# Performance work log

Measured on AMD Instinct MI355X. Metric: run time of the kernel, lower is better.

## Reference

```python
import jax, jax.numpy as jnp
import numpy as np

B, S, H, NH = 8, 1024, 1024, 16
HD = H // NH


def setup_inputs() -> dict:
    key = jax.random.key(0)
    ks = jax.random.split(key, 9)
    scale = 0.02
    d = {"x": jax.random.normal(ks[0], (B, S, H), jnp.float32)}
    for i, n in enumerate(["q", "k", "v", "o"]):
        d["W" + n] = jax.random.normal(ks[1 + i], (H, H), jnp.float32) * scale
        d["b" + n] = jnp.zeros((H,), jnp.float32)
    d["position_idx"] = jnp.arange(S, dtype=jnp.int32).reshape(1, S)
    return d


def _rotate_half(x):
    x1, x2 = jnp.split(x, 2, axis=-1)
    return jnp.concatenate([-x2, x1], axis=-1)


def _apply_rope(x, position_idx):
    # Faithful to source (precedence bug included): (10000**arange) / head_dim
    inv_freq = 1.0 / (10000.0 ** jnp.arange(0, HD, 2, dtype=jnp.float32) / HD)
    freqs = jnp.einsum('bi,j->bij', position_idx.astype(jnp.float32), inv_freq)  # [1,S,HD/2]
    emb = jnp.concatenate([freqs, freqs], axis=-1)  # [1,S,HD]
    cos = jnp.cos(emb).reshape(1, 1, -1, HD)
    sin = jnp.sin(emb).reshape(1, 1, -1, HD)
    return x * cos + _rotate_half(x) * sin


def reference(x, Wq, bq, Wk, bk, Wv, bv, Wo, bo, position_idx):
    b, s, _ = x.shape

    def to_heads(t):  # [b,s,H] -> [b,nh,s,hd]
        return t.reshape(b, s, NH, HD).transpose(0, 2, 1, 3)

    q = to_heads(x @ Wq + bq)
    k = to_heads(x @ Wk + bk)
    v = to_heads(x @ Wv + bv)
    q = _apply_rope(q, position_idx)
    k = _apply_rope(k, position_idx)
    scores = jnp.einsum('bhqd,bhkd->bhqk', q, k) / jnp.sqrt(jnp.float32(HD))
    attn = jax.nn.softmax(scores, axis=-1)
    out = jnp.einsum('bhqk,bhkd->bhqd', attn, v)  # [b,nh,s,hd]
    out = out.transpose(0, 2, 1, 3).reshape(b, s, NH * HD)
    return out @ Wo + bo
```

## Files before the change

### kernel.cpp

```cpp
#include <hip/hip_runtime.h>
#include <hip/hip_bf16.h>
#include <math.h>

#define B_  8
#define S_  1024
#define H_  1024
#define NH_ 16
#define HD_ 64
#define M_  (B_*S_)
#define K_  1024

typedef __hip_bfloat16 bf16;
typedef __attribute__((ext_vector_type(8))) short  short8;
typedef __attribute__((ext_vector_type(4))) short  short4v;
typedef __attribute__((ext_vector_type(8))) __bf16 bf16x8;
typedef __attribute__((ext_vector_type(4))) float  f32x4;

#define MFMA16(a, b, c) __builtin_amdgcn_mfma_f32_16x16x32_bf16((a), (b), (c), 0, 0, 0)
#define QSCALE 0.18033688011112042f

static __device__ __forceinline__ short f2bf_s(float f) {
  unsigned u = __float_as_uint(f);
  u += 0x7fffu + ((u >> 16) & 1u);
  return (short)(u >> 16);
}
static __device__ __forceinline__ float bf2f_s(short s) {
  return __uint_as_float((unsigned)(unsigned short)s << 16);
}

static __device__ __forceinline__ void gload16(const void* g, void* l) {
  __builtin_amdgcn_global_load_lds(
      (const __attribute__((address_space(1))) void*)g,
      (__attribute__((address_space(3))) void*)l, 16, 0, 0);
}

__global__ __launch_bounds__(256) void convert_x_kernel(const float* __restrict__ x,
                                                        short* __restrict__ xb) {
  int i = blockIdx.x * 256 + threadIdx.x;
  size_t base = (size_t)i * 8;
  f32x4 a = *(const f32x4*)(x + base);
  f32x4 b = *(const f32x4*)(x + base + 4);
  short8 v;
  #pragma unroll
  for (int j = 0; j < 4; ++j) { v[j] = f2bf_s(a[j]); v[4 + j] = f2bf_s(b[j]); }
  *(short8*)(xb + base) = v;
}

__global__ void ingest_bias_kernel(const float* __restrict__ b0, const float* __restrict__ b1,
                                   const float* __restrict__ b2, const float* __restrict__ b3,
                                   short* __restrict__ bbuf) {
  int i = blockIdx.x * 256 + threadIdx.x;
  if (i >= 4096) return;
  const float* src = (i < 1024) ? b0 : (i < 2048) ? b1 : (i < 3072) ? b2 : b3;
  bbuf[i] = f2bf_s(src[i & 1023]);
}

__global__ void rope_tables_kernel(const int* __restrict__ pos,
                                   float* __restrict__ cost, float* __restrict__ sint) {
  int i = blockIdx.x * blockDim.x + threadIdx.x;
  if (i >= S_ * 32) return;
  int s = i >> 5, f = i & 31;
  double inv = 64.0 / pow(10000.0, (double)(2 * f));
  double ang = (double)pos[s] * inv;
  cost[i] = (float)cos(ang);
  sint[i] = (float)sin(ang);
}

__global__ __launch_bounds__(256) void transpose_w_kernel(
    const float* __restrict__ w0, const float* __restrict__ w1,
    const float* __restrict__ w2, const float* __restrict__ w3,
    bf16* __restrict__ outbase) {
  const float* src = (blockIdx.y == 0) ? w0 : (blockIdx.y == 1) ? w1 : (blockIdx.y == 2) ? w2 : w3;
  short* dst = (short*)outbase + (size_t)blockIdx.y * H_ * H_;
  __shared__ short tile[64][72];
  const int t = threadIdx.x;
  const int tr = blockIdx.x >> 4, tc = blockIdx.x & 15;
  const int r0 = tr * 64, c0 = tc * 64;
  #pragma unroll
  for (int p = 0; p < 2; ++p) {
    int row = p * 32 + (t >> 3);
    int c8  = (t & 7) * 8;
    const float* f = src + (size_t)(r0 + row) * H_ + c0 + c8;
    #pragma unroll
    for (int j = 0; j < 8; ++j) tile[c8 + j][row] = f2bf_s(f[j]);
  }
  __syncthreads();
  #pragma unroll
  for (int p = 0; p < 2; ++p) {
    int row = p * 32 + (t >> 3);
    int c8  = (t & 7) * 8;
    short8 v;
    #pragma unroll
    for (int j = 0; j < 8; ++j) v[j] = tile[row][c8 + j];
    *(short8*)(dst + (size_t)(c0 + row) * H_ + r0 + c8) = v;
  }
}

__global__ __launch_bounds__(256) void gemm_bt_kernel(
    const bf16* __restrict__ A, const bf16* __restrict__ Bt, const short* __restrict__ bias,
    void* __restrict__ C, const float* __restrict__ cost, const float* __restrict__ sint,
    int mode, float qscale) {
  __shared__ short sA[128 * 32];
  __shared__ short sB[128 * 32];
  const int t  = threadIdx.x;
  const int bm = blockIdx.y * 128, bn = blockIdx.x * 128;
  const int lane = t & 63, wid = t >> 6;
  const int wr = wid >> 1, wc = wid & 1;
  const int lm = lane & 15, lg = lane >> 4;
  f32x4 acc[4][4] = {};

  const short* Ag = (const short*)A;
  const short* Bg = (const short*)Bt;

  for (int k0 = 0; k0 < K_; k0 += 32) {
    #pragma unroll
    for (int c = 0; c < 2; ++c) {
      int flat = c * 256 + t;
      int row = flat >> 2, k8 = (flat & 3) * 8;
      gload16(Ag + (size_t)(bm + row) * K_ + k0 + k8, sA + flat * 8);
      gload16(Bg + (size_t)(bn + row) * K_ + k0 + k8, sB + flat * 8);
    }
    __syncthreads();
    bf16x8 af[4], bfr[4];
    #pragma unroll
    for (int i = 0; i < 4; ++i) af[i]  = *(const bf16x8*)(sA + (wr * 64 + i * 16 + lm) * 32 + lg * 8);
    #pragma unroll
    for (int j = 0; j < 4; ++j) bfr[j] = *(const bf16x8*)(sB + (wc * 64 + j * 16 + lm) * 32 + lg * 8);
    #pragma unroll
    for (int i = 0; i < 4; ++i)
      #pragma unroll
      for (int j = 0; j < 4; ++j)
        acc[i][j] = MFMA16(af[i], bfr[j], acc[i][j]);
    __syncthreads();
  }

  if (mode == 0) {
    #pragma unroll
    for (int i = 0; i < 4; ++i) {
      int row = bm + wr * 64 + i * 16 + lg * 4;
      #pragma unroll
      for (int j = 0; j < 4; ++j) {
        int col = bn + wc * 64 + j * 16 + lm;
        float bv = bf2f_s(bias[col]);
        #pragma unroll
        for (int r = 0; r < 4; ++r)
          ((float*)C)[(size_t)(row + r) * H_ + col] = acc[i][j][r] + bv;
      }
    }
  } else if (mode == 1) {
    #pragma unroll
    for (int i = 0; i < 4; ++i) {
      int row = bm + wr * 64 + i * 16 + lg * 4;
      #pragma unroll
      for (int j = 0; j < 2; ++j) {
        int col0 = bn + wc * 64 + j * 16 + lm;
        int d = col0 & 63;
        float b0 = bf2f_s(bias[col0]);
        float b1 = bf2f_s(bias[col0 + 32]);
        #pragma unroll
        for (int r = 0; r < 4; ++r) {
          int s = (row + r) & (S_ - 1);
          float cv = cost[s * 32 + d] * qscale, sv = sint[s * 32 + d] * qscale;
          float x1 = acc[i][j][r] + b0;
          float x2 = acc[i][j + 2][r] + b1;
          ((short*)C)[(size_t)(row + r) * H_ + col0]      = f2bf_s(x1 * cv - x2 * sv);
          ((short*)C)[(size_t)(row + r) * H_ + col0 + 32] = f2bf_s(x2 * cv + x1 * sv);
        }
      }
    }
  } else {
    #pragma unroll
    for (int i = 0; i < 4; ++i) {
      int row = bm + wr * 64 + i * 16 + lg * 4;
      int bb = row >> 10;
      int sb = row & 1023;
      int pos = (sb & ~31) | (((sb >> 2) & 3) << 3) | (((sb >> 4) & 1) << 2);
      #pragma unroll
      for (int j = 0; j < 4; ++j) {
        int col = bn + wc * 64 + j * 16 + lm;
        int colv = col & 1023;
        float bv = bf2f_s(bias[col]);
        short4v pk;
        #pragma unroll
        for (int r = 0; r < 4; ++r) pk[r] = f2bf_s(acc[i][j][r] + bv);
        short* dstp = (short*)C + ((size_t)(bb * NH_ + (colv >> 6)) * HD_ + (colv & 63)) * S_ + pos;
        *(short4v*)dstp = pk;
      }
    }
  }
}

__global__ __launch_bounds__(256) void attn_kernel(
    const bf16* __restrict__ q, const bf16* __restrict__ k,
    const bf16* __restrict__ vt, bf16* __restrict__ o) {
  const int bh = blockIdx.x, b = bh >> 4, h = bh & 15;
  const int t = threadIdx.x, wid = t >> 6, lane = t & 63;
  const int lm = lane & 15, lg = lane >> 4;
  const int qw = blockIdx.y * 128 + wid * 32;

  __shared__ short sK[2][32 * 64];
  __shared__ short sV[2][64 * 32];

  const int keyr = t >> 3, ccK = t & 7, tcK = ccK ^ (keyr & 7);
  const int dr   = t >> 2, ccV = t & 3, tcV = ccV ^ (dr & 3);
  const short* ksrc = (const short*)k + (size_t)(b * S_ + keyr) * H_ + h * HD_ + tcK * 8;
  const short* vsrc = (const short*)vt + (size_t)bh * HD_ * S_ + (size_t)dr * S_ + tcV * 8;

  const int kO0 = lm * 64 + ((lg ^ (lm & 7)) << 3);
  const int kO1 = lm * 64 + (((4 + lg) ^ (lm & 7)) << 3);
  const int vO  = lm * 32 + ((lg ^ (lm & 3)) << 3);

  const short* qbase = (const short*)q + (size_t)(b * S_ + qw) * H_ + h * HD_;
  bf16x8 qf[2][2];
  #pragma unroll
  for (int mi = 0; mi < 2; ++mi)
    #pragma unroll
    for (int dh = 0; dh < 2; ++dh)
      qf[mi][dh] = *(const bf16x8*)(qbase + (size_t)(mi * 16 + lm) * H_ + dh * 32 + lg * 8);

  float ps[2] = {0.f, 0.f};
  f32x4 oacc[2][4] = {};

  gload16(ksrc, sK[0] + t * 8);
  gload16(vsrc, sV[0] + t * 8);
  __syncthreads();

  int cur = 0;
  for (int kk = 0; kk < S_; kk += 32) {
    if (kk + 32 < S_) {
      gload16(ksrc + (size_t)(kk + 32) * H_, sK[cur ^ 1] + t * 8);
      gload16(vsrc + (kk + 32), sV[cur ^ 1] + t * 8);
    }
    const short* sKc = sK[cur];
    const short* sVc = sV[cur];

    f32x4 sc[2][2] = {};
    #pragma unroll
    for (int nt = 0; nt < 2; ++nt) {
      bf16x8 kf0 = *(const bf16x8*)(sKc + nt * 16 * 64 + kO0);
      bf16x8 kf1 = *(const bf16x8*)(sKc + nt * 16 * 64 + kO1);
      #pragma unroll
      for (int mi = 0; mi < 2; ++mi) {
        sc[mi][nt] = MFMA16(kf0, qf[mi][0], sc[mi][nt]);
        sc[mi][nt] = MFMA16(kf1, qf[mi][1], sc[mi][nt]);
      }
    }
    bf16x8 vf[4];
    #pragma unroll
    for (int dt = 0; dt < 4; ++dt)
      vf[dt] = *(const bf16x8*)(sVc + dt * 16 * 32 + vO);

    bf16x8 pf[2];
    #pragma unroll
    for (int mi = 0; mi < 2; ++mi)
      #pragma unroll
      for (int nt = 0; nt < 2; ++nt)
        #pragma unroll
        for (int r = 0; r < 4; ++r) {
          float p = exp2f(fminf(sc[mi][nt][r], 115.0f));
          ps[mi] += p;
          pf[mi][nt * 4 + r] = (__bf16)p;
        }
    #pragma unroll
    for (int mi = 0; mi < 2; ++mi)
      #pragma unroll
      for (int dt = 0; dt < 4; ++dt)
        oacc[mi][dt] = MFMA16(pf[mi], vf[dt], oacc[mi][dt]);

    __syncthreads();
    cur ^= 1;
  }
  #pragma unroll
  for (int mi = 0; mi < 2; ++mi) {
    ps[mi] += __shfl_xor(ps[mi], 16);
    ps[mi] += __shfl_xor(ps[mi], 32);
  }
  #pragma unroll
  for (int mi = 0; mi < 2; ++mi) {
    #pragma unroll
    for (int r = 0; r < 4; ++r) {
      float rr = 1.0f / __shfl(ps[mi], lg * 4 + r);
      int row = qw + mi * 16 + lg * 4 + r;
      #pragma unroll
      for (int dt = 0; dt < 4; ++dt) {
        int col = h * HD_ + dt * 16 + lm;
        ((short*)o)[(size_t)(b * S_ + row) * H_ + col] = f2bf_s(oacc[mi][dt][r] * rr);
      }
    }
  }
}

extern "C" void kernel_launch(void* const* d_in, const int* in_sizes, int n_in,
                              void* d_out, int out_size, void* d_ws, size_t ws_size,
                              hipStream_t stream) {
  (void)out_size; (void)ws_size;
  int ix, iWq, iWk, iWv, iWo, ibq, ibk, ibv, ibo, ipos;
  const int XS = 8388608, WS = 1048576;
  if (n_in == 10 && in_sizes[0] == WS && in_sizes[9] == XS) {
    iWk = 0; iWo = 1; iWq = 2; iWv = 3; ibk = 4; ibo = 5; ibq = 6; ibv = 7; ipos = 8; ix = 9;
  } else if (n_in == 10 && in_sizes[0] == 1024 && in_sizes[9] == XS) {
    ipos = 0; ibo = 1; iWo = 2; ibv = 3; iWv = 4; ibk = 5; iWk = 6; ibq = 7; iWq = 8; ix = 9;
  } else if (n_in == 10 && in_sizes[0] == XS && in_sizes[1] == 1024) {
    ix = 0; ipos = 1; ibv = 2; ibq = 3; ibo = 4; ibk = 5; iWv = 6; iWq = 7; iWo = 8; iWk = 9;
  } else {
    ix = 0; iWq = 1; ibq = 2; iWk = 3; ibk = 4; iWv = 5; ibv = 6; iWo = 7; ibo = 8; ipos = 9;
  }
  const float* x  = (const float*)d_in[ix];
  const float* Wq = (const float*)d_in[iWq];
  const float* bq = (const float*)d_in[ibq];
  const float* Wk = (const float*)d_in[iWk];
  const float* bk = (const float*)d_in[ibk];
  const float* Wv = (const float*)d_in[iWv];
  const float* bv = (const float*)d_in[ibv];
  const float* Wo = (const float*)d_in[iWo];
  const float* bo = (const float*)d_in[ibo];
  const int*  pos = (const int*)d_in[ipos];

  char* ws = (char*)d_ws;
  bf16* wt    = (bf16*)(ws);
  bf16* kb    = (bf16*)(ws + (8ull  << 20));
  bf16* vtb   = (bf16*)(ws + (24ull << 20));
  bf16* obuf  = (bf16*)(ws + (40ull << 20));
  float* cost = (float*)(ws + (40ull << 20));
  float* sint = (float*)(ws + (40ull << 20) + (size_t)S_ * 32 * sizeof(float));
  short* bbuf = (short*)(ws + (56ull << 20));
  bf16* qb    = (bf16*)d_out;
  short* xb   = (short*)((char*)d_out + (16ull << 20));

  const int NEL = H_ * H_;
  rope_tables_kernel<<<dim3(128), 256, 0, stream>>>(pos, cost, sint);
  ingest_bias_kernel<<<dim3(16), 256, 0, stream>>>(bq, bk, bv, bo, bbuf);
  transpose_w_kernel<<<dim3(256, 4), 256, 0, stream>>>(Wq, Wk, Wv, Wo, wt);
  convert_x_kernel<<<dim3(4096), 256, 0, stream>>>(x, xb);
  gemm_bt_kernel<<<dim3(8, 64), 256, 0, stream>>>((const bf16*)xb, wt + 0 * NEL, bbuf + 0,
                                                  qb,  cost, sint, 1, QSCALE);
  gemm_bt_kernel<<<dim3(8, 64), 256, 0, stream>>>((const bf16*)xb, wt + 1 * NEL, bbuf + 1024,
                                                  kb,  cost, sint, 1, 1.0f);
  gemm_bt_kernel<<<dim3(8, 64), 256, 0, stream>>>((const bf16*)xb, wt + 2 * NEL, bbuf + 2048,
                                                  vtb, cost, sint, 2, 1.0f);
  attn_kernel<<<dim3(128, 8), 256, 0, stream>>>(qb, kb, vtb, obuf);
  gemm_bt_kernel<<<dim3(8, 64), 256, 0, stream>>>(obuf, wt + 3 * NEL, bbuf + 3072,
                                                  d_out, cost, sint, 0, 1.0f);
}
```

Baseline: 202.1 us.

## Deepen GEMM K-tile to 64 with XOR-swizzled LDS, shrink attention query tile

The GEMM now stages 64-wide K slices per iteration with an XOR swizzle on the LDS column chunks. This halves the number of barrier pairs and is meant to cut bank conflicts on the fragment reads. The attention kernel now gives each wave 16 query rows instead of 32 and launches twice as many blocks, raising parallelism and lowering register use, but each block re-reads K/V for fewer queries. The exp clamp at 115 was also removed, which drops a min per element but risks overflow if scores get large.

```diff
diff --git a/kernel.cpp b/kernel.cpp
--- a/kernel.cpp
+++ b/kernel.cpp
@@ -100,8 +100,8 @@
     const bf16* __restrict__ A, const bf16* __restrict__ Bt, const short* __restrict__ bias,
     void* __restrict__ C, const float* __restrict__ cost, const float* __restrict__ sint,
     int mode, float qscale) {
-  __shared__ short sA[128 * 32];
-  __shared__ short sB[128 * 32];
+  __shared__ short sA[128 * 64];
+  __shared__ short sB[128 * 64];
   const int t  = threadIdx.x;
   const int bm = blockIdx.y * 128, bn = blockIdx.x * 128;
   const int lane = t & 63, wid = t >> 6;
@@ -112,25 +112,35 @@
   const short* Ag = (const short*)A;
   const short* Bg = (const short*)Bt;
 
-  for (int k0 = 0; k0 < K_; k0 += 32) {
-    #pragma unroll
-    for (int c = 0; c < 2; ++c) {
+  for (int k0 = 0; k0 < K_; k0 += 64) {
+    #pragma unroll
+    for (int c = 0; c < 4; ++c) {
       int flat = c * 256 + t;
-      int row = flat >> 2, k8 = (flat & 3) * 8;
-      gload16(Ag + (size_t)(bm + row) * K_ + k0 + k8, sA + flat * 8);
-      gload16(Bg + (size_t)(bn + row) * K_ + k0 + k8, sB + flat * 8);
+      int row = flat >> 3, cc = flat & 7;
+      int gcol = (cc ^ (row & 7)) * 8;
+      gload16(Ag + (size_t)(bm + row) * K_ + k0 + gcol, sA + flat * 8);
+      gload16(Bg + (size_t)(bn + row) * K_ + k0 + gcol, sB + flat * 8);
     }
     __syncthreads();
-    bf16x8 af[4], bfr[4];
-    #pragma unroll
-    for (int i = 0; i < 4; ++i) af[i]  = *(const bf16x8*)(sA + (wr * 64 + i * 16 + lm) * 32 + lg * 8);
-    #pragma unroll
-    for (int j = 0; j < 4; ++j) bfr[j] = *(const bf16x8*)(sB + (wc * 64 + j * 16 + lm) * 32 + lg * 8);
-    #pragma unroll
-    for (int i = 0; i < 4; ++i)
-      #pragma unroll
-      for (int j = 0; j < 4; ++j)
-        acc[i][j] = MFMA16(af[i], bfr[j], acc[i][j]);
+    #pragma unroll
+    for (int kk2 = 0; kk2 < 2; ++kk2) {
+      bf16x8 af[4], bfr[4];
+      #pragma unroll
+      for (int i = 0; i < 4; ++i) {
+        int row = wr * 64 + i * 16 + lm;
+        af[i] = *(const bf16x8*)(sA + row * 64 + (((kk2 << 2) + lg) ^ (row & 7)) * 8);
+      }
+      #pragma unroll
+      for (int j = 0; j < 4; ++j) {
+        int row = wc * 64 + j * 16 + lm;
+        bfr[j] = *(const bf16x8*)(sB + row * 64 + (((kk2 << 2) + lg) ^ (row & 7)) * 8);
+      }
+      #pragma unroll
+      for (int i = 0; i < 4; ++i)
+        #pragma unroll
+        for (int j = 0; j < 4; ++j)
+          acc[i][j] = MFMA16(af[i], bfr[j], acc[i][j]);
+    }
     __syncthreads();
   }
 
@@ -196,7 +206,7 @@
   const int bh = blockIdx.x, b = bh >> 4, h = bh & 15;
   const int t = threadIdx.x, wid = t >> 6, lane = t & 63;
   const int lm = lane & 15, lg = lane >> 4;
-  const int qw = blockIdx.y * 128 + wid * 32;
+  const int qw = blockIdx.y * 64 + wid * 16;
 
   __shared__ short sK[2][32 * 64];
   __shared__ short sV[2][64 * 32];
@@ -211,15 +221,11 @@
   const int vO  = lm * 32 + ((lg ^ (lm & 3)) << 3);
 
   const short* qbase = (const short*)q + (size_t)(b * S_ + qw) * H_ + h * HD_;
-  bf16x8 qf[2][2];
-  #pragma unroll
-  for (int mi = 0; mi < 2; ++mi)
-    #pragma unroll
-    for (int dh = 0; dh < 2; ++dh)
-      qf[mi][dh] = *(const bf16x8*)(qbase + (size_t)(mi * 16 + lm) * H_ + dh * 32 + lg * 8);
-
-  float ps[2] = {0.f, 0.f};
-  f32x4 oacc[2][4] = {};
+  bf16x8 qf0 = *(const bf16x8*)(qbase + (size_t)lm * H_ + lg * 8);
+  bf16x8 qf1 = *(const bf16x8*)(qbase + (size_t)lm * H_ + 32 + lg * 8);
+
+  float ps = 0.f;
+  f32x4 oacc[4] = {};
 
   gload16(ksrc, sK[0] + t * 8);
   gload16(vsrc, sV[0] + t * 8);
@@ -234,58 +240,50 @@
     const short* sKc = sK[cur];
     const short* sVc = sV[cur];
 
-    f32x4 sc[2][2] = {};
-    #pragma unroll
-    for (int nt = 0; nt < 2; ++nt) {
-      bf16x8 kf0 = *(const bf16x8*)(sKc + nt * 16 * 64 + kO0);
-      bf16x8 kf1 = *(const bf16x8*)(sKc + nt * 16 * 64 + kO1);
-      #pragma unroll
-      for (int mi = 0; mi < 2; ++mi) {
-        sc[mi][nt] = MFMA16(kf0, qf[mi][0], sc[mi][nt]);
-        sc[mi][nt] = MFMA16(kf1, qf[mi][1], sc[mi][nt]);
-      }
+    f32x4 sc0 = {}, sc1 = {};
+    {
+      bf16x8 kf0 = *(const bf16x8*)(sKc + kO0);
+      bf16x8 kf1 = *(const bf16x8*)(sKc + kO1);
+      sc0 = MFMA16(kf0, qf0, sc0);
+      sc0 = MFMA16(kf1, qf1, sc0);
+    }
+    {
+      bf16x8 kf0 = *(const bf16x8*)(sKc + 16 * 64 + kO0);
+      bf16x8 kf1 = *(const bf16x8*)(sKc + 16 * 64 + kO1);
+      sc1 = MFMA16(kf0, qf0, sc1);
+      sc1 = MFMA16(kf1, qf1, sc1);
     }
     bf16x8 vf[4];
     #pragma unroll
     for (int dt = 0; dt < 4; ++dt)
       vf[dt] = *(const bf16x8*)(sVc + dt * 16 * 32 + vO);
 
-    bf16x8 pf[2];
-    #pragma unroll
-    for (int mi = 0; mi < 2; ++mi)
-      #pragma unroll
-      for (int nt = 0; nt < 2; ++nt)
-        #pragma unroll
-        for (int r = 0; r < 4; ++r) {
-          float p = exp2f(fminf(sc[mi][nt][r], 115.0f));
-          ps[mi] += p;
-          pf[mi][nt * 4 + r] = (__bf16)p;
-        }
-    #pragma unroll
-    for (int mi = 0; mi < 2; ++mi)
-      #pragma unroll
-      for (int dt = 0; dt < 4; ++dt)
-        oacc[mi][dt] = MFMA16(pf[mi], vf[dt], oacc[mi][dt]);
+    bf16x8 pf;
+    #pragma unroll
+    for (int r = 0; r < 4; ++r) {
+      float p0 = exp2f(sc0[r]);
+      float p1 = exp2f(sc1[r]);
+      ps += p0 + p1;
+      pf[r]     = (__bf16)p0;
+      pf[4 + r] = (__bf16)p1;
+    }
+    #pragma unroll
+    for (int dt = 0; dt < 4; ++dt)
+      oacc[dt] = MFMA16(pf, vf[dt], oacc[dt]);
 
     __syncthreads();
     cur ^= 1;
   }
+  ps += __shfl_xor(ps, 16);
+  ps += __shfl_xor(ps, 32);
   #pragma unroll
-  for (int mi = 0; mi < 2; ++mi) {
-    ps[mi] += __shfl_xor(ps[mi], 16);
-    ps[mi] += __shfl_xor(ps[mi], 32);
-  }
-  #pragma unroll
-  for (int mi = 0; mi < 2; ++mi) {
-    #pragma unroll
-    for (int r = 0; r < 4; ++r) {
-      float rr = 1.0f / __shfl(ps[mi], lg * 4 + r);
-      int row = qw + mi * 16 + lg * 4 + r;
-      #pragma unroll
-      for (int dt = 0; dt < 4; ++dt) {
-        int col = h * HD_ + dt * 16 + lm;
-        ((short*)o)[(size_t)(b * S_ + row) * H_ + col] = f2bf_s(oacc[mi][dt][r] * rr);
-      }
+  for (int r = 0; r < 4; ++r) {
+    float rr = 1.0f / __shfl(ps, lg * 4 + r);
+    int row = qw + lg * 4 + r;
+    #pragma unroll
+    for (int dt = 0; dt < 4; ++dt) {
+      int col = h * HD_ + dt * 16 + lm;
+      ((short*)o)[(size_t)(b * S_ + row) * H_ + col] = f2bf_s(oacc[dt][r] * rr);
     }
   }
 }
@@ -338,7 +336,7 @@
                                                   kb,  cost, sint, 1, 1.0f);
   gemm_bt_kernel<<<dim3(8, 64), 256, 0, stream>>>((const bf16*)xb, wt + 2 * NEL, bbuf + 2048,
                                                   vtb, cost, sint, 2, 1.0f);
-  attn_kernel<<<dim3(128, 8), 256, 0, stream>>>(qb, kb, vtb, obuf);
+  attn_kernel<<<dim3(128, 16), 256, 0, stream>>>(qb, kb, vtb, obuf);
   gemm_bt_kernel<<<dim3(8, 64), 256, 0, stream>>>(obuf, wt + 3 * NEL, bbuf + 3072,
                                                   d_out, cost, sint, 0, 1.0f);
 }
```

Result: faster. 195.7 us (-3.2%).

## Deepen GEMM K-tile with XOR-swizzled LDS and double attention queries per warp

Applied to the files above, without the earlier changes.

The GEMM now stages 64-wide K slices into LDS with an XOR swizzle on the 16-byte chunk index. This halves the number of barriers per K and is meant to avoid LDS bank conflicts on fragment reads. The attention kernel gives each wave 64 query rows instead of 32, so every K/V tile loaded into LDS is reused across more queries, and the grid shrinks to 512 blocks. It also drops the exp2 overflow clamp. The changes raise register pressure and reduce the number of attention blocks, and removing the clamp could overflow on large scores.

```diff
diff --git a/kernel.cpp b/kernel.cpp
--- a/kernel.cpp
+++ b/kernel.cpp
@@ -100,8 +100,8 @@
     const bf16* __restrict__ A, const bf16* __restrict__ Bt, const short* __restrict__ bias,
     void* __restrict__ C, const float* __restrict__ cost, const float* __restrict__ sint,
     int mode, float qscale) {
-  __shared__ short sA[128 * 32];
-  __shared__ short sB[128 * 32];
+  __shared__ short sA[128 * 64];
+  __shared__ short sB[128 * 64];
   const int t  = threadIdx.x;
   const int bm = blockIdx.y * 128, bn = blockIdx.x * 128;
   const int lane = t & 63, wid = t >> 6;
@@ -112,25 +112,35 @@
   const short* Ag = (const short*)A;
   const short* Bg = (const short*)Bt;
 
-  for (int k0 = 0; k0 < K_; k0 += 32) {
-    #pragma unroll
-    for (int c = 0; c < 2; ++c) {
+  for (int k0 = 0; k0 < K_; k0 += 64) {
+    #pragma unroll
+    for (int c = 0; c < 4; ++c) {
       int flat = c * 256 + t;
-      int row = flat >> 2, k8 = (flat & 3) * 8;
-      gload16(Ag + (size_t)(bm + row) * K_ + k0 + k8, sA + flat * 8);
-      gload16(Bg + (size_t)(bn + row) * K_ + k0 + k8, sB + flat * 8);
+      int row = flat >> 3, cc = flat & 7;
+      int gcol = (cc ^ (row & 7)) * 8;
+      gload16(Ag + (size_t)(bm + row) * K_ + k0 + gcol, sA + flat * 8);
+      gload16(Bg + (size_t)(bn + row) * K_ + k0 + gcol, sB + flat * 8);
     }
     __syncthreads();
-    bf16x8 af[4], bfr[4];
-    #pragma unroll
-    for (int i = 0; i < 4; ++i) af[i]  = *(const bf16x8*)(sA + (wr * 64 + i * 16 + lm) * 32 + lg * 8);
-    #pragma unroll
-    for (int j = 0; j < 4; ++j) bfr[j] = *(const bf16x8*)(sB + (wc * 64 + j * 16 + lm) * 32 + lg * 8);
-    #pragma unroll
-    for (int i = 0; i < 4; ++i)
-      #pragma unroll
-      for (int j = 0; j < 4; ++j)
-        acc[i][j] = MFMA16(af[i], bfr[j], acc[i][j]);
+    #pragma unroll
+    for (int kk2 = 0; kk2 < 2; ++kk2) {
+      bf16x8 af[4], bfr[4];
+      #pragma unroll
+      for (int i = 0; i < 4; ++i) {
+        int row = wr * 64 + i * 16 + lm;
+        af[i] = *(const bf16x8*)(sA + row * 64 + (((kk2 << 2) + lg) ^ (row & 7)) * 8);
+      }
+      #pragma unroll
+      for (int j = 0; j < 4; ++j) {
+        int row = wc * 64 + j * 16 + lm;
+        bfr[j] = *(const bf16x8*)(sB + row * 64 + (((kk2 << 2) + lg) ^ (row & 7)) * 8);
+      }
+      #pragma unroll
+      for (int i = 0; i < 4; ++i)
+        #pragma unroll
+        for (int j = 0; j < 4; ++j)
+          acc[i][j] = MFMA16(af[i], bfr[j], acc[i][j]);
+    }
     __syncthreads();
   }
 
@@ -196,7 +206,7 @@
   const int bh = blockIdx.x, b = bh >> 4, h = bh & 15;
   const int t = threadIdx.x, wid = t >> 6, lane = t & 63;
   const int lm = lane & 15, lg = lane >> 4;
-  const int qw = blockIdx.y * 128 + wid * 32;
+  const int qw = blockIdx.y * 256 + wid * 64;
 
   __shared__ short sK[2][32 * 64];
   __shared__ short sV[2][64 * 32];
@@ -211,15 +221,15 @@
   const int vO  = lm * 32 + ((lg ^ (lm & 3)) << 3);
 
   const short* qbase = (const short*)q + (size_t)(b * S_ + qw) * H_ + h * HD_;
-  bf16x8 qf[2][2];
-  #pragma unroll
-  for (int mi = 0; mi < 2; ++mi)
+  bf16x8 qf[4][2];
+  #pragma unroll
+  for (int mi = 0; mi < 4; ++mi)
     #pragma unroll
     for (int dh = 0; dh < 2; ++dh)
       qf[mi][dh] = *(const bf16x8*)(qbase + (size_t)(mi * 16 + lm) * H_ + dh * 32 + lg * 8);
 
-  float ps[2] = {0.f, 0.f};
-  f32x4 oacc[2][4] = {};
+  float ps[4] = {};
+  f32x4 oacc[4][4] = {};
 
   gload16(ksrc, sK[0] + t * 8);
   gload16(vsrc, sV[0] + t * 8);
@@ -234,15 +244,16 @@
     const short* sKc = sK[cur];
     const short* sVc = sV[cur];
 
-    f32x4 sc[2][2] = {};
+    f32x4 sc[4][2];
     #pragma unroll
     for (int nt = 0; nt < 2; ++nt) {
       bf16x8 kf0 = *(const bf16x8*)(sKc + nt * 16 * 64 + kO0);
       bf16x8 kf1 = *(const bf16x8*)(sKc + nt * 16 * 64 + kO1);
       #pragma unroll
-      for (int mi = 0; mi < 2; ++mi) {
-        sc[mi][nt] = MFMA16(kf0, qf[mi][0], sc[mi][nt]);
-        sc[mi][nt] = MFMA16(kf1, qf[mi][1], sc[mi][nt]);
+      for (int mi = 0; mi < 4; ++mi) {
+        f32x4 z = {};
+        z = MFMA16(kf0, qf[mi][0], z);
+        sc[mi][nt] = MFMA16(kf1, qf[mi][1], z);
       }
     }
     bf16x8 vf[4];
@@ -250,19 +261,19 @@
     for (int dt = 0; dt < 4; ++dt)
       vf[dt] = *(const bf16x8*)(sVc + dt * 16 * 32 + vO);
 
-    bf16x8 pf[2];
-    #pragma unroll
-    for (int mi = 0; mi < 2; ++mi)
+    bf16x8 pf[4];
+    #pragma unroll
+    for (int mi = 0; mi < 4; ++mi)
       #pragma unroll
       for (int nt = 0; nt < 2; ++nt)
         #pragma unroll
         for (int r = 0; r < 4; ++r) {
-          float p = exp2f(fminf(sc[mi][nt][r], 115.0f));
+          float p = exp2f(sc[mi][nt][r]);
           ps[mi] += p;
           pf[mi][nt * 4 + r] = (__bf16)p;
         }
     #pragma unroll
-    for (int mi = 0; mi < 2; ++mi)
+    for (int mi = 0; mi < 4; ++mi)
       #pragma unroll
       for (int dt = 0; dt < 4; ++dt)
         oacc[mi][dt] = MFMA16(pf[mi], vf[dt], oacc[mi][dt]);
@@ -271,12 +282,12 @@
     cur ^= 1;
   }
   #pragma unroll
-  for (int mi = 0; mi < 2; ++mi) {
+  for (int mi = 0; mi < 4; ++mi) {
     ps[mi] += __shfl_xor(ps[mi], 16);
     ps[mi] += __shfl_xor(ps[mi], 32);
   }
   #pragma unroll
-  for (int mi = 0; mi < 2; ++mi) {
+  for (int mi = 0; mi < 4; ++mi) {
     #pragma unroll
     for (int r = 0; r < 4; ++r) {
       float rr = 1.0f / __shfl(ps[mi], lg * 4 + r);
@@ -338,7 +349,7 @@
                                                   kb,  cost, sint, 1, 1.0f);
   gemm_bt_kernel<<<dim3(8, 64), 256, 0, stream>>>((const bf16*)xb, wt + 2 * NEL, bbuf + 2048,
                                                   vtb, cost, sint, 2, 1.0f);
-  attn_kernel<<<dim3(128, 8), 256, 0, stream>>>(qb, kb, vtb, obuf);
+  attn_kernel<<<dim3(128, 4), 256, 0, stream>>>(qb, kb, vtb, obuf);
   gemm_bt_kernel<<<dim3(8, 64), 256, 0, stream>>>(obuf, wt + 3 * NEL, bbuf + 3072,
                                                   d_out, cost, sint, 0, 1.0f);
 }
```

Result: faster. 187.3 us (-7.3%).
